# Kernel tuning notes

Measured on AMD Instinct MI355X. Metric: run time of the kernel, lower is better.

## Reference

```python
import jax, jax.numpy as jnp
import numpy as np

IN_FEATURES = 5000
N0, N1, N2 = 512, 512, 256   # num_nodes; encoder: in->N0->N2 (skips N1), decoder: N2->N1->N0->2*in
NUM_TREATMENTS = 20
BATCH = 8192
TREAT_COLS = 2


def _glorot(key, shape):
    fan_in, fan_out = shape[-2], shape[-1]
    lim = np.sqrt(6.0 / (fan_in + fan_out)).astype(np.float32)
    return jax.random.uniform(key, shape, jnp.float32, -lim, lim)


def setup_inputs() -> dict:
    key = jax.random.key(0)
    ks = jax.random.split(key, 12)
    inp = {
        "input": jax.random.normal(ks[0], (BATCH, IN_FEATURES), jnp.float32),
        "treatment": jax.random.randint(ks[1], (BATCH, TREAT_COLS), 0, NUM_TREATMENTS + 1),
        # encoder: in -> N0 -> N2 (both layers ReLU)
        "enc_W1": _glorot(ks[2], (IN_FEATURES, N0)),
        "enc_b1": jnp.zeros((N0,), jnp.float32),
        "enc_W2": _glorot(ks[3], (N0, N2)),
        "enc_b2": jnp.zeros((N2,), jnp.float32),
        # per-treatment single layers: N2 -> N2, ReLU
        "T_W": _glorot(ks[4], (NUM_TREATMENTS, N2, N2)),
        "T_b": jnp.zeros((NUM_TREATMENTS, N2), jnp.float32),
        # decoder: N2 -> N1 -> N0 -> 2*in (last layer linear)
        "dec_W1": _glorot(ks[5], (N2, N1)),
        "dec_b1": jnp.zeros((N1,), jnp.float32),
        "dec_W2": _glorot(ks[6], (N1, N0)),
        "dec_b2": jnp.zeros((N0,), jnp.float32),
        "dec_W3": _glorot(ks[7], (N0, 2 * IN_FEATURES)),
        "dec_b3": jnp.zeros((2 * IN_FEATURES,), jnp.float32),
    }
    return inp


def reference(input, treatment, enc_W1, enc_b1, enc_W2, enc_b2, T_W, T_b,
              dec_W1, dec_b1, dec_W2, dec_b2, dec_W3, dec_b3):
    dim = input.shape[1]
    # encoder
    h = jax.nn.relu(input @ enc_W1 + enc_b1)
    embedding = jax.nn.relu(h @ enc_W2 + enc_b2)            # [B, N2]

    # per-treatment dispatch, vectorized over experts
    tvals = jnp.arange(1, NUM_TREATMENTS + 1)               # treatments are 1-indexed
    mask = jnp.any(treatment[None, :, :] == tvals[:, None, None], axis=-1)  # [T, B] bool
    # original skips a treatment unless more than one sample is assigned to it
    apply_t = jnp.sum(mask, axis=1) > 1                     # [T]
    gate = (mask & apply_t[:, None]).astype(embedding.dtype)  # [T, B]

    expert_out = jax.nn.relu(jnp.einsum('bd,tde->tbe', embedding, T_W) + T_b[:, None, :])  # [T, B, N2]
    latent_rep = jnp.einsum('tbe,tb->be', expert_out, gate)  # scatter-add of masked experts

    # decoder
    h = jax.nn.relu(latent_rep @ dec_W1 + dec_b1)
    h = jax.nn.relu(h @ dec_W2 + dec_b2)
    rec = h @ dec_W3 + dec_b3                               # [B, 2*dim]

    gene_means = rec[:, :dim]
    gene_vars = jax.nn.softplus(rec[:, dim:]) + 0.001
    return jnp.concatenate([gene_means, gene_vars], axis=1)
```

## Files before the change

kernel.cpp:

```cpp
#include <hip/hip_runtime.h>
#include <hip/hip_bf16.h>
#include <hip/hip_fp16.h>
#include <math.h>

#define BATCH 8192
#define IN_F 5000
#define KP1 5024
#define NN0 512
#define NN1 512
#define NN2 256
#define NTREAT 20
#define OUTF (2*IN_F)
#define NP3 10240

typedef _Float16 f16;
typedef _Float16 f16x8 __attribute__((ext_vector_type(8)));
typedef float f32x4 __attribute__((ext_vector_type(4)));
typedef __attribute__((address_space(3))) void as3_void;
typedef const __attribute__((address_space(1))) void cas1_void;

__device__ __forceinline__ int fswz(int row) { return (row >> 1) & 3; }

__device__ __forceinline__ float softplusf(float x) {
    return fmaxf(x, 0.f) + log1pf(expf(-fabsf(x)));
}

__global__ void zero64_kernel(int* __restrict__ p) {
    if (threadIdx.x < 64) p[threadIdx.x] = 0;
}
__global__ void count_kernel(const int* __restrict__ treat, int* __restrict__ cnt) {
    int b = blockIdx.x * blockDim.x + threadIdx.x;
    if (b >= BATCH) return;
    int t0 = treat[2*b], t1 = treat[2*b+1];
    if (t0 >= 1 && t0 <= NTREAT) atomicAdd(&cnt[t0], 1);
    if (t1 >= 1 && t1 <= NTREAT && t1 != t0) atomicAdd(&cnt[t1], 1);
}
__global__ void pair_kernel(const int* __restrict__ treat, const int* __restrict__ cnt,
                            int* __restrict__ epair) {
    int b = blockIdx.x * blockDim.x + threadIdx.x;
    if (b >= BATCH) return;
    int t0 = treat[2*b], t1 = treat[2*b+1];
    int e0 = (t0 >= 1 && t0 <= NTREAT && cnt[t0] > 1) ? (t0 - 1) : -1;
    int e1 = (t1 >= 1 && t1 <= NTREAT && t1 != t0 && cnt[t1] > 1) ? (t1 - 1) : -1;
    epair[2*b] = e0;
    epair[2*b+1] = e1;
}
__global__ void scatter_kernel(const int* __restrict__ epair, int* __restrict__ pos,
                               int* __restrict__ rows) {
    int b = blockIdx.x * blockDim.x + threadIdx.x;
    if (b >= BATCH) return;
    #pragma unroll
    for (int p = 0; p < 2; ++p) {
        int t = epair[2*b + p];
        if (t >= 0) {
            int x = atomicAdd(&pos[t], 1);
            rows[t * BATCH + x] = b * 2 + p;
        }
    }
}

__global__ __launch_bounds__(256) void convw_kernel(
    const float* __restrict__ W, f16* __restrict__ Whi, f16* __restrict__ Wlo,
    int K, int N, int Kp) {
    __shared__ float t[64][65];
    const int k0 = blockIdx.x * 64;
    const int n0 = blockIdx.y * 64;
    const int tid = threadIdx.x;
    #pragma unroll
    for (int i = 0; i < 16; ++i) {
        int idx = tid + i*256;
        int r = idx >> 6, c = idx & 63;
        float v = 0.f;
        if (k0 + r < K && n0 + c < N) v = W[(size_t)(k0+r)*N + n0 + c];
        t[r][c] = v;
    }
    __syncthreads();
    const int n = tid >> 2;
    const int q0 = (tid & 3) * 2;
    const int f = fswz(n0 + n);
    #pragma unroll
    for (int h = 0; h < 2; ++h) {
        int q = q0 + h;
        if (k0 + q*8 >= Kp) continue;
        f16x8 hv, lv;
        #pragma unroll
        for (int j = 0; j < 8; ++j) {
            float x = t[q*8 + j][n];
            f16 hi = (f16)x;
            hv[j] = hi;
            lv[j] = (f16)(x - (float)hi);
        }
        size_t base = (size_t)(n0 + n) * Kp + (size_t)(k0 + (((q & 3) ^ f) << 3) + (q >> 2) * 32);
        *(f16x8*)&Whi[base] = hv;
        *(f16x8*)&Wlo[base] = lv;
    }
}

__global__ __launch_bounds__(256) void expert_gemm(
    const float* __restrict__ emb, const float* __restrict__ T_W,
    const float* __restrict__ T_b, const int* __restrict__ pos,
    const int* __restrict__ rows, float* __restrict__ latA, float* __restrict__ latB) {
    const int t = blockIdx.x;
    const int n = pos[t];
    const int base = blockIdx.y * 16;
    if (base >= n) return;
    const int nr = min(16, n - base);
    __shared__ float se[16][256];
    __shared__ int ridx[16];
    const int tid = threadIdx.x;
    if (tid < 16) ridx[tid] = (tid < nr) ? rows[t * BATCH + base + tid] : 0;
    __syncthreads();
    #pragma unroll
    for (int s = 0; s < 16; ++s)
        se[s][tid] = (s < nr) ? emb[(size_t)(ridx[s] >> 1) * NN2 + tid] : 0.f;
    __syncthreads();
    float acc[16];
    const float bcol = T_b[t * NN2 + tid];
    #pragma unroll
    for (int s = 0; s < 16; ++s) acc[s] = bcol;
    const float* W = T_W + (size_t)t * NN2 * NN2 + tid;
    for (int d0 = 0; d0 < NN2; d0 += 4) {
        float w0 = W[(size_t)(d0+0) * NN2];
        float w1 = W[(size_t)(d0+1) * NN2];
        float w2 = W[(size_t)(d0+2) * NN2];
        float w3 = W[(size_t)(d0+3) * NN2];
        #pragma unroll
        for (int s = 0; s < 16; ++s) {
            float4 e = *(const float4*)&se[s][d0];
            acc[s] = fmaf(e.x, w0, fmaf(e.y, w1, fmaf(e.z, w2, fmaf(e.w, w3, acc[s]))));
        }
    }
    for (int s = 0; s < nr; ++s) {
        int rp = ridx[s];
        float* dst = (rp & 1) ? latB : latA;
        dst[(size_t)(rp >> 1) * NN2 + tid] = fmaxf(acc[s], 0.f);
    }
}

__global__ __launch_bounds__(256) void latconv_kernel(
    const float* __restrict__ latA, const float* __restrict__ latB,
    f16* __restrict__ lhi, f16* __restrict__ llo) {
    const int idx = blockIdx.x * 256 + threadIdx.x;
    const int m = idx >> 8, k = idx & 255;
    float v = latA[idx] + latB[idx];
    f16 hi = (f16)v;
    size_t o = (size_t)m * NN2 + (size_t)(k ^ (fswz(m) << 3));
    lhi[o] = hi;
    llo[o] = (f16)(v - (float)hi);
}

template<int MODE, bool XCVT, int BN, int BM = 256>
__global__ __launch_bounds__((BM == 128) ? 256 : 512, 2) void gemm8(
    const f16* __restrict__ Xhi, const f16* __restrict__ Xlo,
    const float* __restrict__ X32, int ldx,
    const f16* __restrict__ Whi, const f16* __restrict__ Wlo,
    const float* __restrict__ bias,
    float* __restrict__ C32, f16* __restrict__ Chi, f16* __restrict__ Clo,
    int Kp, int K_real, int N_real, int NpOut, int halfN) {
    constexpr int NTH = (BM == 128) ? 256 : 512;
    constexpr int NWAVE = NTH / 64;
    constexpr int WN_WAVES = (BN == 256) ? 4 : 2;
    constexpr int WM_WAVES = NWAVE / WN_WAVES;
    constexpr int WMT = BM / WM_WAVES;
    constexpr int WNT = BN / WN_WAVES;
    constexpr int MF = WMT / 16;
    constexpr int NF = WNT / 16;
    constexpr int XSZ = BM * 32;
    constexpr int WSZ = BN * 32;
    constexpr int GLL = (BN == 64) ? 5 : 8;
    __shared__ f16 lds[2][2*XSZ + 2*WSZ];

    const int tid = threadIdx.x;
    const int wid = tid >> 6;
    const int lane = tid & 63;
    const int lr = lane & 15;
    const int ls = lane >> 4;
    const int m0 = blockIdx.y * BM;
    const int n0 = blockIdx.x * BN;
    const int wm = (wid / WN_WAVES) * WMT;
    const int wn = (wid % WN_WAVES) * WNT;
    const int koff = ((ls ^ ((lr >> 1) & 3)) << 3);
    const int nk = Kp / 32;

    f32x4 acc[MF][NF] = {};

    auto stage = [&](int bi, int kt) {
        f16* Xh = lds[bi];
        f16* Xl = Xh + XSZ;
        f16* Wh = Xl + XSZ;
        f16* Wl = Wh + WSZ;
        const int kk = kt * 32 + (lane & 3) * 8;
        const int rlo = lane >> 2;
        if constexpr (BN == 128) {
            #pragma unroll
            for (int c = 0; c < 2; ++c) {
                const int rb = wid * 32 + c * 16;
                const size_t g = (size_t)(n0 + rb + rlo) * Kp + kk;
                __builtin_amdgcn_global_load_lds((cas1_void*)(Whi + g), (as3_void*)(Wh + rb*32), 16, 0, 0);
                __builtin_amdgcn_global_load_lds((cas1_void*)(Wlo + g), (as3_void*)(Wl + rb*32), 16, 0, 0);
            }
        } else {
            const int rb = (wid & 3) * 16;
            const size_t g = (size_t)(n0 + rb + rlo) * Kp + kk;
            const f16* src = (wid < 4) ? (Whi + g) : (Wlo + g);
            f16* dst = ((wid < 4) ? Wh : Wl) + rb*32;
            __builtin_amdgcn_global_load_lds((cas1_void*)src, (as3_void*)dst, 16, 0, 0);
        }
        if constexpr (!XCVT) {
            if constexpr (BM == 256) {
                #pragma unroll
                for (int c = 0; c < 2; ++c) {
                    const int rb = c * 128 + wid * 16;
                    const size_t g = (size_t)(m0 + rb + rlo) * Kp + kk;
                    __builtin_amdgcn_global_load_lds((cas1_void*)(Xhi + g), (as3_void*)(Xh + rb*32), 16, 0, 0);
                    __builtin_amdgcn_global_load_lds((cas1_void*)(Xlo + g), (as3_void*)(Xl + rb*32), 16, 0, 0);
                }
            } else {
                #pragma unroll
                for (int c = 0; c < 2; ++c) {
                    const int rb = wid * 32 + c * 16;
                    const size_t g = (size_t)(m0 + rb + rlo) * Kp + kk;
                    __builtin_amdgcn_global_load_lds((cas1_void*)(Xhi + g), (as3_void*)(Xh + rb*32), 16, 0, 0);
                    __builtin_amdgcn_global_load_lds((cas1_void*)(Xlo + g), (as3_void*)(Xl + rb*32), 16, 0, 0);
                }
            }
        } else {
            const int ar = tid >> 1;
            const int q0 = (tid & 1) * 2;
            const int fr = fswz(ar);
            const int k0 = kt * 32;
            const float* ap = X32 + (size_t)(m0 + ar) * ldx + (size_t)(k0 + q0 * 8);
            float v[16];
            if (k0 + 32 <= K_real) {
                float4 u0 = *(const float4*)(ap);
                float4 u1 = *(const float4*)(ap + 4);
                float4 u2 = *(const float4*)(ap + 8);
                float4 u3 = *(const float4*)(ap + 12);
                v[0]=u0.x; v[1]=u0.y; v[2]=u0.z; v[3]=u0.w;
                v[4]=u1.x; v[5]=u1.y; v[6]=u1.z; v[7]=u1.w;
                v[8]=u2.x; v[9]=u2.y; v[10]=u2.z; v[11]=u2.w;
                v[12]=u3.x; v[13]=u3.y; v[14]=u3.z; v[15]=u3.w;
            } else {
                #pragma unroll
                for (int j2 = 0; j2 < 16; ++j2) {
                    int kk2 = k0 + q0*8 + j2;
                    v[j2] = (kk2 < K_real) ? X32[(size_t)(m0 + ar) * ldx + kk2] : 0.f;
                }
            }
            #pragma unroll
            for (int h2 = 0; h2 < 2; ++h2) {
                f16x8 hv, lv;
                #pragma unroll
                for (int j2 = 0; j2 < 8; ++j2) {
                    float x = v[h2*8 + j2];
                    f16 hh = (f16)x;
                    hv[j2] = hh;
                    lv[j2] = (f16)(x - (float)hh);
                }
                const int dst = ar*32 + (((q0 + h2) ^ fr) << 3);
                *(f16x8*)&Xh[dst] = hv;
                *(f16x8*)&Xl[dst] = lv;
            }
        }
    };

    if constexpr (!XCVT) {
        stage(0, 0);
        stage(1, 1);
        for (int t = 0; t < nk; ++t) {
            if (t + 1 < nk) {
                asm volatile("s_waitcnt vmcnt(%0)" :: "i"(GLL) : "memory");
            } else {
                asm volatile("s_waitcnt vmcnt(0)" ::: "memory");
            }
            __builtin_amdgcn_s_barrier();
            const f16* Xh = lds[t & 1];
            const f16* Xl = Xh + XSZ;
            const f16* Wh = Xl + XSZ;
            const f16* Wl = Wh + WSZ;
            f16x8 bh[NF], bl[NF], ah[MF], al[MF];
            #pragma unroll
            for (int j = 0; j < NF; ++j) {
                const int r = (wn + j*16 + lr) * 32 + koff;
                bh[j] = *(const f16x8*)&Wh[r];
                bl[j] = *(const f16x8*)&Wl[r];
            }
            #pragma unroll
            for (int i = 0; i < MF; ++i) {
                const int r = (wm + i*16 + lr) * 32 + koff;
                ah[i] = *(const f16x8*)&Xh[r];
                al[i] = *(const f16x8*)&Xl[r];
            }
            asm volatile("s_waitcnt lgkmcnt(0)" ::: "memory");
            __builtin_amdgcn_sched_barrier(0);
            __builtin_amdgcn_s_barrier();
            if (t + 2 < nk) stage(t & 1, t + 2);
            __builtin_amdgcn_s_setprio(1);
            #pragma unroll
            for (int i = 0; i < MF; ++i)
                #pragma unroll
                for (int j = 0; j < NF; ++j)
                    acc[i][j] = __builtin_amdgcn_mfma_f32_16x16x32_f16(ah[i], bh[j], acc[i][j], 0, 0, 0);
            #pragma unroll
            for (int i = 0; i < MF; ++i)
                #pragma unroll
                for (int j = 0; j < NF; ++j)
                    acc[i][j] = __builtin_amdgcn_mfma_f32_16x16x32_f16(ah[i], bl[j], acc[i][j], 0, 0, 0);
            #pragma unroll
            for (int i = 0; i < MF; ++i)
                #pragma unroll
                for (int j = 0; j < NF; ++j)
                    acc[i][j] = __builtin_amdgcn_mfma_f32_16x16x32_f16(al[i], bh[j], acc[i][j], 0, 0, 0);
            __builtin_amdgcn_s_setprio(0);
        }
    } else {
        stage(0, 0);
        __syncthreads();
        for (int t = 0; t < nk; ++t) {
            if (t + 1 < nk) stage((t + 1) & 1, t + 1);
            const f16* Xh = lds[t & 1];
            const f16* Xl = Xh + XSZ;
            const f16* Wh = Xl + XSZ;
            const f16* Wl = Wh + WSZ;
            f16x8 bh[NF], bl[NF];
            #pragma unroll
            for (int j = 0; j < NF; ++j) {
                const int r = (wn + j*16 + lr) * 32 + koff;
                bh[j] = *(const f16x8*)&Wh[r];
                bl[j] = *(const f16x8*)&Wl[r];
            }
            __builtin_amdgcn_s_setprio(1);
            #pragma unroll
            for (int ih = 0; ih < MF; ih += 4) {
                f16x8 ah[4], al[4];
                #pragma unroll
                for (int i = 0; i < 4; ++i) {
                    const int r = (wm + (ih + i)*16 + lr) * 32 + koff;
                    ah[i] = *(const f16x8*)&Xh[r];
                    al[i] = *(const f16x8*)&Xl[r];
                }
                #pragma unroll
                for (int i = 0; i < 4; ++i)
                    #pragma unroll
                    for (int j = 0; j < NF; ++j)
                        acc[ih+i][j] = __builtin_amdgcn_mfma_f32_16x16x32_f16(ah[i], bh[j], acc[ih+i][j], 0, 0, 0);
                #pragma unroll
                for (int i = 0; i < 4; ++i)
                    #pragma unroll
                    for (int j = 0; j < NF; ++j)
                        acc[ih+i][j] = __builtin_amdgcn_mfma_f32_16x16x32_f16(ah[i], bl[j], acc[ih+i][j], 0, 0, 0);
                #pragma unroll
                for (int i = 0; i < 4; ++i)
                    #pragma unroll
                    for (int j = 0; j < NF; ++j)
                        acc[ih+i][j] = __builtin_amdgcn_mfma_f32_16x16x32_f16(al[i], bh[j], acc[ih+i][j], 0, 0, 0);
            }
            __builtin_amdgcn_s_setprio(0);
            __syncthreads();
        }
    }

    #pragma unroll
    for (int i = 0; i < MF; ++i) {
        #pragma unroll
        for (int j = 0; j < NF; ++j) {
            const int col = n0 + wn + j*16 + lr;
            if (col >= N_real) continue;
            const float bcol = bias[col];
            #pragma unroll
            for (int q = 0; q < 4; ++q) {
                const int m = m0 + wm + i*16 + ls*4 + q;
                float vv = acc[i][j][q] + bcol;
                if (MODE == 0) {
                    C32[(size_t)m * N_real + col] = fmaxf(vv, 0.f);
                } else if (MODE == 1) {
                    vv = fmaxf(vv, 0.f);
                    f16 hi = (f16)vv;
                    const size_t idx = (size_t)m * NpOut + (size_t)(col ^ (fswz(m) << 3));
                    Chi[idx] = hi;
                    Clo[idx] = (f16)(vv - (float)hi);
                } else {
                    if (col >= halfN) vv = softplusf(vv) + 0.001f;
                    C32[(size_t)m * N_real + col] = vv;
                }
            }
        }
    }
}

extern "C" void kernel_launch(void* const* d_in, const int* in_sizes, int n_in,
                              void* d_out, int out_size, void* d_ws, size_t ws_size,
                              hipStream_t stream) {
    const float* input  = (const float*)d_in[0];
    const int*   treat  = (const int*)d_in[1];
    const float* enc_W1 = (const float*)d_in[2];
    const float* enc_b1 = (const float*)d_in[3];
    const float* enc_W2 = (const float*)d_in[4];
    const float* enc_b2 = (const float*)d_in[5];
    const float* T_W    = (const float*)d_in[6];
    const float* T_b    = (const float*)d_in[7];
    const float* dec_W1 = (const float*)d_in[8];
    const float* dec_b1 = (const float*)d_in[9];
    const float* dec_W2 = (const float*)d_in[10];
    const float* dec_b2 = (const float*)d_in[11];
    const float* dec_W3 = (const float*)d_in[12];
    const float* dec_b3 = (const float*)d_in[13];
    float* out = (float*)d_out;

    uint8_t* p = (uint8_t*)d_ws;
    f16* h1hi = (f16*)p;  float* latA = (float*)p;  p += (size_t)BATCH*NN0*2;
    f16* h1lo = (f16*)p;  float* latB = (float*)p;  p += (size_t)BATCH*NN0*2;
    float* emb = (float*)p;  f16* h4hi = (f16*)p;   p += (size_t)BATCH*NN2*4;
    f16* lathi = (f16*)p;  f16* h4lo = (f16*)p;     p += (size_t)BATCH*NN2*2;
    f16* latlo = (f16*)p;                           p += (size_t)BATCH*NN2*2;
    f16* w1hi = (f16*)p;               p += (size_t)NN0*KP1*2;
    f16* w1lo = (f16*)p;               p += (size_t)NN0*KP1*2;
    f16* w2hi = (f16*)p;               p += (size_t)NN2*NN0*2;
    f16* w2lo = (f16*)p;               p += (size_t)NN2*NN0*2;
    f16* dw1hi = (f16*)p;              p += (size_t)NN1*NN2*2;
    f16* dw1lo = (f16*)p;              p += (size_t)NN1*NN2*2;
    f16* dw2hi = (f16*)p;              p += (size_t)NN0*NN1*2;
    f16* dw2lo = (f16*)p;              p += (size_t)NN0*NN1*2;
    f16* dw3hi = (f16*)p;              p += (size_t)NP3*NN0*2;
    f16* dw3lo = (f16*)p;              p += (size_t)NP3*NN0*2;
    int* cnt   = (int*)p;              p += 32*4;
    int* pos   = (int*)p;              p += 32*4;
    int* epair = (int*)p;              p += (size_t)BATCH*2*4;
    int* rows  = (int*)p;              p += (size_t)NTREAT*BATCH*4;
    f16* h3hi = h1hi;
    f16* h3lo = h1lo;

    zero64_kernel<<<1, 64, 0, stream>>>(cnt);
    count_kernel<<<BATCH/256, 256, 0, stream>>>(treat, cnt);
    pair_kernel<<<BATCH/256, 256, 0, stream>>>(treat, cnt, epair);
    scatter_kernel<<<BATCH/256, 256, 0, stream>>>(epair, pos, rows);

    convw_kernel<<<dim3((KP1+63)/64, NN0/64), 256, 0, stream>>>(enc_W1, w1hi, w1lo, IN_F, NN0, KP1);
    convw_kernel<<<dim3(NN0/64, NN2/64), 256, 0, stream>>>(enc_W2, w2hi, w2lo, NN0, NN2, NN0);
    convw_kernel<<<dim3(NN2/64, NN1/64), 256, 0, stream>>>(dec_W1, dw1hi, dw1lo, NN2, NN1, NN2);
    convw_kernel<<<dim3(NN1/64, NN0/64), 256, 0, stream>>>(dec_W2, dw2hi, dw2lo, NN1, NN0, NN1);
    convw_kernel<<<dim3(NN0/64, NP3/64), 256, 0, stream>>>(dec_W3, dw3hi, dw3lo, NN0, OUTF, NN0);

    gemm8<1, true, 64><<<dim3(NN0/64, BATCH/256), 512, 0, stream>>>(
        nullptr, nullptr, input, IN_F, w1hi, w1lo, enc_b1,
        nullptr, h1hi, h1lo, KP1, IN_F, NN0, NN0, 0);
    gemm8<0, false, 64><<<dim3(NN2/64, BATCH/256), 512, 0, stream>>>(
        h1hi, h1lo, nullptr, 0, w2hi, w2lo, enc_b2,
        emb, nullptr, nullptr, NN0, NN0, NN2, NN2, 0);
    hipMemsetAsync(latA, 0, (size_t)BATCH*NN2*4*2, stream);
    expert_gemm<<<dim3(NTREAT, BATCH/16), 256, 0, stream>>>(emb, T_W, T_b, pos, rows, latA, latB);
    latconv_kernel<<<BATCH*NN2/256, 256, 0, stream>>>(latA, latB, lathi, latlo);
    gemm8<1, false, 64><<<dim3(NN1/64, BATCH/256), 512, 0, stream>>>(
        lathi, latlo, nullptr, 0, dw1hi, dw1lo, dec_b1,
        nullptr, h3hi, h3lo, NN2, NN2, NN1, NN1, 0);
    gemm8<1, false, 64><<<dim3(NN0/64, BATCH/256), 512, 0, stream>>>(
        h3hi, h3lo, nullptr, 0, dw2hi, dw2lo, dec_b2,
        nullptr, h4hi, h4lo, NN1, NN1, NN0, NN0, 0);
    gemm8<2, false, 128, 128><<<dim3(NP3/128, BATCH/128), 256, 0, stream>>>(
        h4hi, h4lo, nullptr, 0, dw3hi, dw3lo, dec_b3,
        out, nullptr, nullptr, NN0, NN0, OUTF, OUTF, IN_F);
}
```

Baseline: 932.9 us.

## Overlap LDS low-part loads with high-part MFMAs and swizzle block order

The main GEMM loop now loads the high-half fragments first and issues the low-half LDS reads. It then waits only for the high halves and runs the hi*hi MFMAs while the low-half reads are still in flight, before the barrier and the next stage's prefetch. For MODE 2, which is likely the large decoder output GEMM, it also remaps the linear block index so that groups of 8 consecutive blocks share tiles, aiming for better L2 reuse. The costs are longer register live ranges and an ordering that relies on hard-coded grid dimensions (80 by 64).

```diff
diff --git a/kernel.cpp b/kernel.cpp
--- a/kernel.cpp
+++ b/kernel.cpp
@@ -175,8 +175,16 @@
     const int lane = tid & 63;
     const int lr = lane & 15;
     const int ls = lane >> 4;
-    const int m0 = blockIdx.y * BM;
-    const int n0 = blockIdx.x * BN;
+    int m0, n0;
+    if constexpr (MODE == 2) {
+        const int lin = blockIdx.y * 80 + blockIdx.x;
+        const int swz = (lin & 7) * 640 + (lin >> 3);
+        m0 = (swz & 63) * BM;
+        n0 = (swz >> 6) * BN;
+    } else {
+        m0 = blockIdx.y * BM;
+        n0 = blockIdx.x * BN;
+    }
     const int wm = (wid / WN_WAVES) * WMT;
     const int wn = (wid % WN_WAVES) * WNT;
     const int koff = ((ls ^ ((lr >> 1) & 3)) << 3);
@@ -280,27 +288,32 @@
             const f16* Wl = Wh + WSZ;
             f16x8 bh[NF], bl[NF], ah[MF], al[MF];
             #pragma unroll
-            for (int j = 0; j < NF; ++j) {
-                const int r = (wn + j*16 + lr) * 32 + koff;
-                bh[j] = *(const f16x8*)&Wh[r];
-                bl[j] = *(const f16x8*)&Wl[r];
-            }
-            #pragma unroll
-            for (int i = 0; i < MF; ++i) {
-                const int r = (wm + i*16 + lr) * 32 + koff;
-                ah[i] = *(const f16x8*)&Xh[r];
-                al[i] = *(const f16x8*)&Xl[r];
-            }
+            for (int j = 0; j < NF; ++j)
+                bh[j] = *(const f16x8*)&Wh[(wn + j*16 + lr) * 32 + koff];
+            #pragma unroll
+            for (int i = 0; i < MF; ++i)
+                ah[i] = *(const f16x8*)&Xh[(wm + i*16 + lr) * 32 + koff];
+            __builtin_amdgcn_sched_barrier(0);
+            #pragma unroll
+            for (int j = 0; j < NF; ++j)
+                bl[j] = *(const f16x8*)&Wl[(wn + j*16 + lr) * 32 + koff];
+            #pragma unroll
+            for (int i = 0; i < MF; ++i)
+                al[i] = *(const f16x8*)&Xl[(wm + i*16 + lr) * 32 + koff];
+            asm volatile("s_waitcnt lgkmcnt(%0)" :: "i"(MF + NF) : "memory");
+            __builtin_amdgcn_sched_barrier(0);
+            __builtin_amdgcn_s_setprio(1);
+            #pragma unroll
+            for (int i = 0; i < MF; ++i)
+                #pragma unroll
+                for (int j = 0; j < NF; ++j)
+                    acc[i][j] = __builtin_amdgcn_mfma_f32_16x16x32_f16(ah[i], bh[j], acc[i][j], 0, 0, 0);
+            __builtin_amdgcn_sched_barrier(0);
             asm volatile("s_waitcnt lgkmcnt(0)" ::: "memory");
             __builtin_amdgcn_sched_barrier(0);
             __builtin_amdgcn_s_barrier();
+            __builtin_amdgcn_sched_barrier(0);
             if (t + 2 < nk) stage(t & 1, t + 2);
-            __builtin_amdgcn_s_setprio(1);
-            #pragma unroll
-            for (int i = 0; i < MF; ++i)
-                #pragma unroll
-                for (int j = 0; j < NF; ++j)
-                    acc[i][j] = __builtin_amdgcn_mfma_f32_16x16x32_f16(ah[i], bh[j], acc[i][j], 0, 0, 0);
             #pragma unroll
             for (int i = 0; i < MF; ++i)
                 #pragma unroll
```

Measured after the change: 1.055 ms. +13.1%, slower.

## Add dedicated 256x256-tile split-f16 GEMM kernel for final decoder layer

Applied to the files above, without the earlier changes.

Replaces the generic 128x128 gemm8 call for the largest decoder GEMM (512 to 10000) with a specialized kernel using 256x256 tiles, 8 waves, and a double-buffered global_load_lds pipeline. Each wave computes its 128x64 sub-tile in quarter phases, interleaving LDS reads and next-tile staging with MFMA bursts under raised priority. The larger tile raises arithmetic intensity and cuts global traffic for the three-term hi/lo f16 emulation of fp32. The cost is more registers and LDS, fewer blocks per CU, and many barriers per K step.

```diff
diff --git a/kernel.cpp b/kernel.cpp
--- a/kernel.cpp
+++ b/kernel.cpp
@@ -388,6 +388,214 @@
     }
 }
 
+__global__ __launch_bounds__(512, 2) void gemm_dec3(
+    const f16* __restrict__ Xhi, const f16* __restrict__ Xlo,
+    const f16* __restrict__ Whi, const f16* __restrict__ Wlo,
+    const float* __restrict__ bias, float* __restrict__ C32) {
+    constexpr int XSZ = 256 * 32;
+    __shared__ f16 lds[2][4 * XSZ];
+
+    const int tid = threadIdx.x;
+    const int wid = tid >> 6;
+    const int lane = tid & 63;
+    const int lr = lane & 15;
+    const int ls = lane >> 4;
+    const int m0 = blockIdx.y * 256;
+    const int n0 = blockIdx.x * 256;
+    const int wm = (wid >> 2) * 128;
+    const int wn = (wid & 3) * 64;
+    const int koff = ((ls ^ ((lr >> 1) & 3)) << 3);
+    const int kk_s = (lane & 3) * 8;
+    const int rlo = lane >> 2;
+
+    f32x4 acc[8][4] = {};
+
+    auto stageX = [&](int bi, int kt) {
+        f16* Xh = lds[bi];
+        f16* Xl = Xh + XSZ;
+        const int kk = kt * 32 + kk_s;
+        #pragma unroll
+        for (int c = 0; c < 2; ++c) {
+            const int rb = c * 128 + wid * 16;
+            const size_t g = (size_t)(m0 + rb + rlo) * NN0 + kk;
+            __builtin_amdgcn_global_load_lds((cas1_void*)(Xhi + g), (as3_void*)(Xh + rb*32), 16, 0, 0);
+            __builtin_amdgcn_global_load_lds((cas1_void*)(Xlo + g), (as3_void*)(Xl + rb*32), 16, 0, 0);
+        }
+    };
+    auto stageW = [&](int bi, int kt) {
+        f16* Wh = lds[bi] + 2 * XSZ;
+        f16* Wl = Wh + XSZ;
+        const int kk = kt * 32 + kk_s;
+        #pragma unroll
+        for (int c = 0; c < 2; ++c) {
+            const int rb = c * 128 + wid * 16;
+            const size_t g = (size_t)(n0 + rb + rlo) * NN0 + kk;
+            __builtin_amdgcn_global_load_lds((cas1_void*)(Whi + g), (as3_void*)(Wh + rb*32), 16, 0, 0);
+            __builtin_amdgcn_global_load_lds((cas1_void*)(Wlo + g), (as3_void*)(Wl + rb*32), 16, 0, 0);
+        }
+    };
+
+    stageX(0, 0);
+    stageW(0, 0);
+    asm volatile("s_waitcnt vmcnt(0)" ::: "memory");
+    __builtin_amdgcn_s_barrier();
+
+    for (int t = 0; t < 16; ++t) {
+        const int cur = t & 1;
+        const f16* Xh = lds[cur];
+        const f16* Xl = Xh + XSZ;
+        const f16* Wh = Xh + 2 * XSZ;
+        const f16* Wl = Xh + 3 * XSZ;
+        f16x8 ah[4], al[4], bh[2], bl[2];
+
+        #pragma unroll
+        for (int i = 0; i < 4; ++i) {
+            const int r = (wm + i*16 + lr) * 32 + koff;
+            ah[i] = *(const f16x8*)&Xh[r];
+            al[i] = *(const f16x8*)&Xl[r];
+        }
+        #pragma unroll
+        for (int j = 0; j < 2; ++j) {
+            const int r = (wn + j*16 + lr) * 32 + koff;
+            bh[j] = *(const f16x8*)&Wh[r];
+            bl[j] = *(const f16x8*)&Wl[r];
+        }
+        if (t + 1 < 16) stageX(cur ^ 1, t + 1);
+        __builtin_amdgcn_s_barrier();
+        asm volatile("s_waitcnt lgkmcnt(0)" ::: "memory");
+        __builtin_amdgcn_sched_barrier(0);
+        __builtin_amdgcn_s_setprio(1);
+        #pragma unroll
+        for (int i = 0; i < 4; ++i)
+            #pragma unroll
+            for (int j = 0; j < 2; ++j)
+                acc[i][j] = __builtin_amdgcn_mfma_f32_16x16x32_f16(ah[i], bh[j], acc[i][j], 0, 0, 0);
+        #pragma unroll
+        for (int i = 0; i < 4; ++i)
+            #pragma unroll
+            for (int j = 0; j < 2; ++j)
+                acc[i][j] = __builtin_amdgcn_mfma_f32_16x16x32_f16(ah[i], bl[j], acc[i][j], 0, 0, 0);
+        #pragma unroll
+        for (int i = 0; i < 4; ++i)
+            #pragma unroll
+            for (int j = 0; j < 2; ++j)
+                acc[i][j] = __builtin_amdgcn_mfma_f32_16x16x32_f16(al[i], bh[j], acc[i][j], 0, 0, 0);
+        __builtin_amdgcn_s_setprio(0);
+        __builtin_amdgcn_s_barrier();
+
+        #pragma unroll
+        for (int j = 0; j < 2; ++j) {
+            const int r = (wn + (j+2)*16 + lr) * 32 + koff;
+            bh[j] = *(const f16x8*)&Wh[r];
+            bl[j] = *(const f16x8*)&Wl[r];
+        }
+        if (t + 1 < 16) stageW(cur ^ 1, t + 1);
+        __builtin_amdgcn_s_barrier();
+        asm volatile("s_waitcnt lgkmcnt(0)" ::: "memory");
+        __builtin_amdgcn_sched_barrier(0);
+        __builtin_amdgcn_s_setprio(1);
+        #pragma unroll
+        for (int i = 0; i < 4; ++i)
+            #pragma unroll
+            for (int j = 0; j < 2; ++j)
+                acc[i][j+2] = __builtin_amdgcn_mfma_f32_16x16x32_f16(ah[i], bh[j], acc[i][j+2], 0, 0, 0);
+        #pragma unroll
+        for (int i = 0; i < 4; ++i)
+            #pragma unroll
+            for (int j = 0; j < 2; ++j)
+                acc[i][j+2] = __builtin_amdgcn_mfma_f32_16x16x32_f16(ah[i], bl[j], acc[i][j+2], 0, 0, 0);
+        #pragma unroll
+        for (int i = 0; i < 4; ++i)
+            #pragma unroll
+            for (int j = 0; j < 2; ++j)
+                acc[i][j+2] = __builtin_amdgcn_mfma_f32_16x16x32_f16(al[i], bh[j], acc[i][j+2], 0, 0, 0);
+        __builtin_amdgcn_s_setprio(0);
+        __builtin_amdgcn_s_barrier();
+
+        #pragma unroll
+        for (int i = 0; i < 4; ++i) {
+            const int r = (wm + (i+4)*16 + lr) * 32 + koff;
+            ah[i] = *(const f16x8*)&Xh[r];
+            al[i] = *(const f16x8*)&Xl[r];
+        }
+        #pragma unroll
+        for (int j = 0; j < 2; ++j) {
+            const int r = (wn + j*16 + lr) * 32 + koff;
+            bh[j] = *(const f16x8*)&Wh[r];
+            bl[j] = *(const f16x8*)&Wl[r];
+        }
+        __builtin_amdgcn_s_barrier();
+        asm volatile("s_waitcnt lgkmcnt(0)" ::: "memory");
+        __builtin_amdgcn_sched_barrier(0);
+        __builtin_amdgcn_s_setprio(1);
+        #pragma unroll
+        for (int i = 0; i < 4; ++i)
+            #pragma unroll
+            for (int j = 0; j < 2; ++j)
+                acc[i+4][j] = __builtin_amdgcn_mfma_f32_16x16x32_f16(ah[i], bh[j], acc[i+4][j], 0, 0, 0);
+        #pragma unroll
+        for (int i = 0; i < 4; ++i)
+            #pragma unroll
+            for (int j = 0; j < 2; ++j)
+                acc[i+4][j] = __builtin_amdgcn_mfma_f32_16x16x32_f16(ah[i], bl[j], acc[i+4][j], 0, 0, 0);
+        #pragma unroll
+        for (int i = 0; i < 4; ++i)
+            #pragma unroll
+            for (int j = 0; j < 2; ++j)
+                acc[i+4][j] = __builtin_amdgcn_mfma_f32_16x16x32_f16(al[i], bh[j], acc[i+4][j], 0, 0, 0);
+        __builtin_amdgcn_s_setprio(0);
+        __builtin_amdgcn_s_barrier();
+
+        #pragma unroll
+        for (int j = 0; j < 2; ++j) {
+            const int r = (wn + (j+2)*16 + lr) * 32 + koff;
+            bh[j] = *(const f16x8*)&Wh[r];
+            bl[j] = *(const f16x8*)&Wl[r];
+        }
+        __builtin_amdgcn_s_barrier();
+        asm volatile("s_waitcnt lgkmcnt(0)" ::: "memory");
+        __builtin_amdgcn_sched_barrier(0);
+        __builtin_amdgcn_s_setprio(1);
+        #pragma unroll
+        for (int i = 0; i < 4; ++i)
+            #pragma unroll
+            for (int j = 0; j < 2; ++j)
+                acc[i+4][j+2] = __builtin_amdgcn_mfma_f32_16x16x32_f16(ah[i], bh[j], acc[i+4][j+2], 0, 0, 0);
+        #pragma unroll
+        for (int i = 0; i < 4; ++i)
+            #pragma unroll
+            for (int j = 0; j < 2; ++j)
+                acc[i+4][j+2] = __builtin_amdgcn_mfma_f32_16x16x32_f16(ah[i], bl[j], acc[i+4][j+2], 0, 0, 0);
+        #pragma unroll
+        for (int i = 0; i < 4; ++i)
+            #pragma unroll
+            for (int j = 0; j < 2; ++j)
+                acc[i+4][j+2] = __builtin_amdgcn_mfma_f32_16x16x32_f16(al[i], bh[j], acc[i+4][j+2], 0, 0, 0);
+        __builtin_amdgcn_s_setprio(0);
+        if (t + 1 < 16) {
+            asm volatile("s_waitcnt vmcnt(0)" ::: "memory");
+        }
+        __builtin_amdgcn_s_barrier();
+    }
+
+    #pragma unroll
+    for (int i = 0; i < 8; ++i) {
+        #pragma unroll
+        for (int j = 0; j < 4; ++j) {
+            const int col = n0 + wn + j*16 + lr;
+            if (col >= OUTF) continue;
+            const float bcol = bias[col];
+            #pragma unroll
+            for (int q = 0; q < 4; ++q) {
+                const int m = m0 + wm + i*16 + ls*4 + q;
+                float vv = acc[i][j][q] + bcol;
+                if (col >= IN_F) vv = softplusf(vv) + 0.001f;
+                C32[(size_t)m * OUTF + col] = vv;
+            }
+        }
+    }
+}
+
 extern "C" void kernel_launch(void* const* d_in, const int* in_sizes, int n_in,
                               void* d_out, int out_size, void* d_ws, size_t ws_size,
                               hipStream_t stream) {
@@ -456,7 +664,6 @@
     gemm8<1, false, 64><<<dim3(NN0/64, BATCH/256), 512, 0, stream>>>(
         h3hi, h3lo, nullptr, 0, dw2hi, dw2lo, dec_b2,
         nullptr, h4hi, h4lo, NN1, NN1, NN0, NN0, 0);
-    gemm8<2, false, 128, 128><<<dim3(NP3/128, BATCH/128), 256, 0, stream>>>(
-        h4hi, h4lo, nullptr, 0, dw3hi, dw3lo, dec_b3,
-        out, nullptr, nullptr, NN0, NN0, OUTF, OUTF, IN_F);
-}
+    gemm_dec3<<<dim3(NP3/256, BATCH/256), 512, 0, stream>>>(
+        h4hi, h4lo, dw3hi, dw3lo, dec_b3, out);
+}
```

Result: slower. 1.161 ms (+24.5%).

## Specialize final decoder GEMM to load A operand directly into registers

Applied to the files above, without the earlier changes.

Adds a dedicated kernel for the last decoder layer that stages only the weight tiles into double-buffered LDS via global_load_lds and reads the activation (A) fragments straight from global memory into registers. The aim is to halve LDS traffic and capacity per block, permitting three blocks per CU, and to raise MFMA priority during the split-f16 (hi/lo) accumulation. The trade-off is that A loads become uncoalesced-by-LDS global reads reissued for each column block, relying on L2 caching, and the softplus epilogue is kept unchanged.

```diff
diff --git a/kernel.cpp b/kernel.cpp
--- a/kernel.cpp
+++ b/kernel.cpp
@@ -383,6 +383,105 @@
                     if (col >= halfN) vv = softplusf(vv) + 0.001f;
                     C32[(size_t)m * N_real + col] = vv;
                 }
+            }
+        }
+    }
+}
+
+__global__ __launch_bounds__(256, 3) void gemm_dec3_areg(
+    const f16* __restrict__ Xhi, const f16* __restrict__ Xlo,
+    const f16* __restrict__ Whi, const f16* __restrict__ Wlo,
+    const float* __restrict__ bias, float* __restrict__ C32) {
+    constexpr int WSZ = 128 * 32;
+    __shared__ f16 lds[2][2 * WSZ];
+
+    const int tid = threadIdx.x;
+    const int wid = tid >> 6;
+    const int lane = tid & 63;
+    const int lr = lane & 15;
+    const int ls = lane >> 4;
+    const int m0 = blockIdx.y * 128;
+    const int n0 = blockIdx.x * 128;
+    const int wm = (wid >> 1) * 64;
+    const int wn = (wid & 1) * 64;
+    const int koff = ((ls ^ ((lr >> 1) & 3)) << 3);
+    const int kk_s = (lane & 3) * 8;
+    const int rlo = lane >> 2;
+
+    const int f_a = (lr >> 1) & 3;
+    size_t arow[4];
+    #pragma unroll
+    for (int i = 0; i < 4; ++i)
+        arow[i] = (size_t)(m0 + wm + i*16 + lr) * NN0 + ((ls ^ f_a) << 3);
+
+    f32x4 acc[4][4] = {};
+
+    auto stageW = [&](int bi, int kt) {
+        f16* Wh = lds[bi];
+        f16* Wl = Wh + WSZ;
+        const int kk = kt * 32 + kk_s;
+        const int rb = wid * 32;
+        #pragma unroll
+        for (int c = 0; c < 2; ++c) {
+            const size_t g = (size_t)(n0 + rb + c*16 + rlo) * NN0 + kk;
+            __builtin_amdgcn_global_load_lds((cas1_void*)(Whi + g), (as3_void*)(Wh + (rb + c*16)*32), 16, 0, 0);
+            __builtin_amdgcn_global_load_lds((cas1_void*)(Wlo + g), (as3_void*)(Wl + (rb + c*16)*32), 16, 0, 0);
+        }
+    };
+
+    stageW(0, 0);
+    __syncthreads();
+    for (int t = 0; t < 16; ++t) {
+        if (t + 1 < 16) stageW((t + 1) & 1, t + 1);
+        f16x8 ah[4], al[4];
+        #pragma unroll
+        for (int i = 0; i < 4; ++i) {
+            const size_t ga = arow[i] + t * 32;
+            ah[i] = *(const f16x8*)(Xhi + ga);
+            al[i] = *(const f16x8*)(Xlo + ga);
+        }
+        const f16* Wh = lds[t & 1];
+        const f16* Wl = Wh + WSZ;
+        f16x8 bh[4], bl[4];
+        #pragma unroll
+        for (int j = 0; j < 4; ++j) {
+            const int r = (wn + j*16 + lr) * 32 + koff;
+            bh[j] = *(const f16x8*)&Wh[r];
+            bl[j] = *(const f16x8*)&Wl[r];
+        }
+        __builtin_amdgcn_s_setprio(1);
+        #pragma unroll
+        for (int i = 0; i < 4; ++i)
+            #pragma unroll
+            for (int j = 0; j < 4; ++j)
+                acc[i][j] = __builtin_amdgcn_mfma_f32_16x16x32_f16(ah[i], bh[j], acc[i][j], 0, 0, 0);
+        #pragma unroll
+        for (int i = 0; i < 4; ++i)
+            #pragma unroll
+            for (int j = 0; j < 4; ++j)
+                acc[i][j] = __builtin_amdgcn_mfma_f32_16x16x32_f16(ah[i], bl[j], acc[i][j], 0, 0, 0);
+        #pragma unroll
+        for (int i = 0; i < 4; ++i)
+            #pragma unroll
+            for (int j = 0; j < 4; ++j)
+                acc[i][j] = __builtin_amdgcn_mfma_f32_16x16x32_f16(al[i], bh[j], acc[i][j], 0, 0, 0);
+        __builtin_amdgcn_s_setprio(0);
+        __syncthreads();
+    }
+
+    #pragma unroll
+    for (int i = 0; i < 4; ++i) {
+        #pragma unroll
+        for (int j = 0; j < 4; ++j) {
+            const int col = n0 + wn + j*16 + lr;
+            if (col >= OUTF) continue;
+            const float bcol = bias[col];
+            #pragma unroll
+            for (int q = 0; q < 4; ++q) {
+                const int m = m0 + wm + i*16 + ls*4 + q;
+                float vv = acc[i][j][q] + bcol;
+                if (col >= IN_F) vv = softplusf(vv) + 0.001f;
+                C32[(size_t)m * OUTF + col] = vv;
             }
         }
     }
@@ -456,7 +555,6 @@
     gemm8<1, false, 64><<<dim3(NN0/64, BATCH/256), 512, 0, stream>>>(
         h3hi, h3lo, nullptr, 0, dw2hi, dw2lo, dec_b2,
         nullptr, h4hi, h4lo, NN1, NN1, NN0, NN0, 0);
-    gemm8<2, false, 128, 128><<<dim3(NP3/128, BATCH/128), 256, 0, stream>>>(
-        h4hi, h4lo, nullptr, 0, dw3hi, dw3lo, dec_b3,
-        out, nullptr, nullptr, NN0, NN0, OUTF, OUTF, IN_F);
-}
+    gemm_dec3_areg<<<dim3(NP3/128, BATCH/128), 256, 0, stream>>>(
+        h4hi, h4lo, dw3hi, dw3lo, dec_b3, out);
+}
```

Result: no change. 921.1 us (-1.3%).
